# Optimization experiments

Hardware: AMD Instinct MI355X
Metric: run time of the kernel (lower is better)

## Reference

```python
import jax, jax.numpy as jnp
import numpy as np

B, T, D, H = 8, 2048, 1024, 128  # batch, seq, input_size, head_size


def setup_inputs() -> dict:
    key = jax.random.key(0)
    kx, kq, kk, kv = jax.random.split(key, 4)
    s = 1.0 / np.sqrt(D)
    return {
        "x": jax.random.normal(kx, (B, T, D), dtype=jnp.float32),
        "Wq": jax.random.normal(kq, (D, H), dtype=jnp.float32) * s,
        "Wk": jax.random.normal(kk, (D, H), dtype=jnp.float32) * s,
        "Wv": jax.random.normal(kv, (D, H), dtype=jnp.float32) * s,
    }


def reference(x, Wq, Wk, Wv):
    # projections (Linear, no bias)
    q = jnp.einsum("btd,dh->bth", x, Wq)
    k = jnp.einsum("btd,dh->bth", x, Wk)
    v = jnp.einsum("btd,dh->bth", x, Wv)
    scale = H ** (-0.5)
    scores = jnp.einsum("bth,bsh->bts", q, k) * scale  # [B,T,T]
    t = x.shape[1]
    causal = jnp.tril(jnp.ones((t, t), dtype=bool))
    scores = jnp.where(causal, scores, -jnp.inf)
    attn = jax.nn.softmax(scores, axis=-1)  # dropout p=0.0 -> identity
    out = jnp.einsum("bts,bsh->bth", attn, v)
    return out
```

## Files before the change

### kernel.cpp

```cpp
#include <hip/hip_runtime.h>
#include <math.h>

#define B_ 8
#define T_ 2048
#define D_ 1024
#define H_ 128
#define BT (B_ * T_)

typedef short bf16x8 __attribute__((ext_vector_type(8)));
typedef float f32x4 __attribute__((ext_vector_type(4)));

static constexpr float SCALE = 0.08838834764831845f;

__device__ inline unsigned short f2b(float f) {
  unsigned int u = __float_as_uint(f);
  u += 0x7FFF + ((u >> 16) & 1);
  return (unsigned short)(u >> 16);
}
__device__ inline unsigned int pk2(float a, float b) {
  return (unsigned int)f2b(a) | ((unsigned int)f2b(b) << 16);
}

__device__ __forceinline__ void gll16(const void* g, void* l) {
  __builtin_amdgcn_global_load_lds(
      (const __attribute__((address_space(1))) void*)g,
      (__attribute__((address_space(3))) void*)l, 16, 0, 0);
}

__global__ __launch_bounds__(256) void wcvt_kernel(
    const float* __restrict__ Wq, const float* __restrict__ Wk,
    const float* __restrict__ Wv, short* __restrict__ Wt) {
  __shared__ short Wls[128 * 72];
  const int sel = blockIdx.y;
  const float* W = sel == 0 ? Wq : (sel == 1 ? Wk : Wv);
  const int d0 = blockIdx.x * 64;
  const int tid = threadIdx.x;
#pragma unroll
  for (int i = 0; i < 8; ++i) {
    int slot = tid + i * 256;
    int r = slot >> 5, hg = slot & 31;
    float4 w = *(const float4*)(W + (size_t)(d0 + r) * H_ + hg * 4);
    Wls[(hg * 4 + 0) * 72 + r] = (short)f2b(w.x);
    Wls[(hg * 4 + 1) * 72 + r] = (short)f2b(w.y);
    Wls[(hg * 4 + 2) * 72 + r] = (short)f2b(w.z);
    Wls[(hg * 4 + 3) * 72 + r] = (short)f2b(w.w);
  }
  __syncthreads();
  short* dst = Wt + (size_t)sel * D_ * H_;
#pragma unroll
  for (int i = 0; i < 4; ++i) {
    int slot = tid + i * 256;
    int h = slot >> 3, g = slot & 7;
    *(int4*)(dst + (size_t)h * D_ + d0 + g * 8) = *(int4*)&Wls[h * 72 + g * 8];
  }
}

__global__ __launch_bounds__(256) void proj_kernel(
    const float* __restrict__ x, const short* __restrict__ Wt,
    short* __restrict__ qb, short* __restrict__ kb, short* __restrict__ vtb) {
  __shared__ alignas(16) char smem[36864];
  short* Xs = (short*)smem;
  short* Ws = (short*)(smem + 16384);

  const int tid = threadIdx.x;
  const int wave = tid >> 6, lane = tid & 63;
  const int ln = lane & 15, quad = lane >> 4;
  const int mw = wave & 1, nw = wave >> 1;
  const int sel = blockIdx.y;
  const int row0 = blockIdx.x * 128;
  const short* W = Wt + (size_t)sel * (size_t)(D_ * H_);

  f32x4 acc[4][4];
#pragma unroll
  for (int mi = 0; mi < 4; ++mi)
#pragma unroll
    for (int ni = 0; ni < 4; ++ni) acc[mi][ni] = (f32x4){0.f, 0.f, 0.f, 0.f};

  for (int s = 0; s < 16; ++s) {
    const int k0 = s * 64;
    if (s) __syncthreads();

#pragma unroll
    for (int j = 0; j < 4; ++j) {
      const int rbase = wave * 32 + j * 8;
      const int n = rbase + (lane >> 3);
      const int gp = (lane & 7) ^ (n & 7);
      gll16(W + (size_t)n * D_ + k0 + gp * 8, (char*)Ws + rbase * 128);
    }
    {
      float4 xr[8];
#pragma unroll
      for (int i = 0; i < 8; ++i) {
        int fid = tid + i * 256;
        int r = fid >> 4, g4 = fid & 15;
        xr[i] = *(const float4*)(x + (size_t)(row0 + r) * D_ + k0 + g4 * 4);
      }
#pragma unroll
      for (int i = 0; i < 8; ++i) {
        int fid = tid + i * 256;
        int r = fid >> 4, g4 = fid & 15;
        int g = g4 >> 1, half = g4 & 1;
        unsigned int* p = (unsigned int*)&Xs[r * 64 + ((g ^ (r & 7)) * 8) + half * 4];
        p[0] = pk2(xr[i].x, xr[i].y);
        p[1] = pk2(xr[i].z, xr[i].w);
      }
    }
    __syncthreads();

#pragma unroll
    for (int kk = 0; kk < 2; ++kk) {
      bf16x8 a[4];
#pragma unroll
      for (int mi = 0; mi < 4; ++mi) {
        int r = mw * 64 + mi * 16 + ln;
        int g = kk * 4 + quad;
        a[mi] = *(bf16x8*)&Xs[r * 64 + ((g ^ (r & 7)) * 8)];
      }
#pragma unroll
      for (int ni = 0; ni < 4; ++ni) {
        int n = nw * 64 + ni * 16 + ln;
        int g = kk * 4 + quad;
        bf16x8 bb = *(bf16x8*)&Ws[n * 64 + ((g ^ (n & 7)) * 8)];
#pragma unroll
        for (int mi = 0; mi < 4; ++mi)
          acc[mi][ni] = __builtin_amdgcn_mfma_f32_16x16x32_bf16(a[mi], bb, acc[mi][ni], 0, 0, 0);
      }
    }
  }

  __syncthreads();
  short* Cs = (short*)smem;
  if (sel < 2) {
    short* out = sel ? kb : qb;
#pragma unroll
    for (int mi = 0; mi < 4; ++mi)
#pragma unroll
      for (int ni = 0; ni < 4; ++ni)
#pragma unroll
        for (int rr = 0; rr < 4; ++rr)
          Cs[(mw * 64 + mi * 16 + quad * 4 + rr) * 136 + nw * 64 + ni * 16 + ln] =
              (short)f2b(acc[mi][ni][rr]);
    __syncthreads();
#pragma unroll
    for (int i = 0; i < 8; ++i) {
      int slot = tid + i * 256;
      int r = slot >> 4, g = slot & 15;
      *(int4*)(out + (size_t)(row0 + r) * H_ + g * 8) = *(int4*)&Cs[r * 136 + g * 8];
    }
  } else {
#pragma unroll
    for (int mi = 0; mi < 4; ++mi)
#pragma unroll
      for (int ni = 0; ni < 4; ++ni)
#pragma unroll
        for (int rr = 0; rr < 4; ++rr)
          Cs[(nw * 64 + ni * 16 + ln) * 136 + mw * 64 + mi * 16 + quad * 4 + rr] =
              (short)f2b(acc[mi][ni][rr]);
    __syncthreads();
    const int b = row0 >> 11, t0 = row0 & 2047;
#pragma unroll
    for (int i = 0; i < 8; ++i) {
      int slot = tid + i * 256;
      int h = slot >> 4, g = slot & 15;
      *(int4*)(vtb + (size_t)(b * H_ + h) * T_ + t0 + g * 8) = *(int4*)&Cs[h * 136 + g * 8];
    }
  }
}

__global__ __launch_bounds__(256) void attn_kernel(
    const short* __restrict__ qb, const short* __restrict__ kb,
    const short* __restrict__ vtb, float* __restrict__ out) {
  __shared__ alignas(16) short Ks[2][64 * 128];
  __shared__ alignas(16) short Vt[2][128 * 64];
  __shared__ alignas(16) float Sf[32 * 65];
  __shared__ alignas(16) short P[32 * 72];
  __shared__ float aA[32], lL[32];

  const int tid = threadIdx.x;
  const int wave = tid >> 6, lane = tid & 63;
  const int ln = lane & 15, quad = lane >> 4;
  const int slot = blockIdx.x & 255;
  const int pass = blockIdx.x >> 8;
  const int b = slot >> 5;
  const int j = slot & 31;
  const int tile = pass ? (63 - j) : j;
  const int q0 = tile * 32;

  bf16x8 qfr[2][4];
#pragma unroll
  for (int m = 0; m < 2; ++m)
#pragma unroll
    for (int kk = 0; kk < 4; ++kk)
      qfr[m][kk] = *(const bf16x8*)(qb + (size_t)(b * T_ + q0 + m * 16 + ln) * H_ +
                                    kk * 32 + quad * 8);

  f32x4 oacc[2][2];
#pragma unroll
  for (int m = 0; m < 2; ++m)
#pragma unroll
    for (int nt = 0; nt < 2; ++nt) oacc[m][nt] = (f32x4){0.f, 0.f, 0.f, 0.f};

  const int srow = tid >> 3, l8 = tid & 7;
  float m_run = -INFINITY, l_run = 0.f;

  auto stage = [&](int bf, int s0) {
#pragma unroll
    for (int jj = 0; jj < 4; ++jj) {
      const int rb = wave * 16 + jj * 4;
      const int r = rb + (lane >> 4);
      const int gp = (lane & 15) ^ (r & 7);
      gll16(kb + (size_t)(b * T_ + s0 + r) * H_ + gp * 8,
            (char*)&Ks[bf][0] + rb * 256);
    }
#pragma unroll
    for (int jj = 0; jj < 4; ++jj) {
      const int hb = wave * 32 + jj * 8;
      const int h = hb + (lane >> 3);
      const int gp = (lane & 7) ^ (h & 7);
      gll16(vtb + (size_t)(b * H_ + h) * T_ + s0 + gp * 8,
            (char*)&Vt[bf][0] + hb * 128);
    }
  };

  const int nch = ((q0 + 31) >> 6) + 1;
  stage(0, 0);

  for (int ch = 0; ch < nch; ++ch) {
    const int cur = ch & 1;
    const int s0 = ch * 64;
    __syncthreads();
    if (ch + 1 < nch) stage(cur ^ 1, s0 + 64);

    f32x4 sacc[2];
    sacc[0] = (f32x4){0.f, 0.f, 0.f, 0.f};
    sacc[1] = (f32x4){0.f, 0.f, 0.f, 0.f};
#pragma unroll
    for (int kk = 0; kk < 4; ++kk) {
      const int r = wave * 16 + ln;
      bf16x8 bk = *(bf16x8*)&Ks[cur][r * 128 + (((kk * 4 + quad) ^ (r & 7)) * 8)];
#pragma unroll
      for (int m = 0; m < 2; ++m)
        sacc[m] = __builtin_amdgcn_mfma_f32_16x16x32_bf16(qfr[m][kk], bk, sacc[m], 0, 0, 0);
    }
#pragma unroll
    for (int m = 0; m < 2; ++m)
#pragma unroll
      for (int r = 0; r < 4; ++r)
        Sf[(m * 16 + quad * 4 + r) * 65 + wave * 16 + ln] = sacc[m][r];
    __syncthreads();

    float sv[8];
    const int qg = q0 + srow;
#pragma unroll
    for (int i = 0; i < 8; ++i) {
      float s = Sf[srow * 65 + l8 * 8 + i] * SCALE;
      sv[i] = (s0 + l8 * 8 + i <= qg) ? s : -INFINITY;
    }
    float mx = sv[0];
#pragma unroll
    for (int i = 1; i < 8; ++i) mx = fmaxf(mx, sv[i]);
    mx = fmaxf(mx, __shfl_xor(mx, 1));
    mx = fmaxf(mx, __shfl_xor(mx, 2));
    mx = fmaxf(mx, __shfl_xor(mx, 4));
    const float mnew = fmaxf(m_run, mx);
    const float alpha = __expf(m_run - mnew);
    float p[8], ps = 0.f;
#pragma unroll
    for (int i = 0; i < 8; ++i) {
      p[i] = __expf(sv[i] - mnew);
      ps += p[i];
    }
    ps += __shfl_xor(ps, 1);
    ps += __shfl_xor(ps, 2);
    ps += __shfl_xor(ps, 4);
    l_run = l_run * alpha + ps;
    m_run = mnew;
    int4 pw;
    pw.x = (int)pk2(p[0], p[1]);
    pw.y = (int)pk2(p[2], p[3]);
    pw.z = (int)pk2(p[4], p[5]);
    pw.w = (int)pk2(p[6], p[7]);
    *(int4*)&P[srow * 72 + l8 * 8] = pw;
    if (l8 == 0) aA[srow] = alpha;
    __syncthreads();

    const int h0 = wave * 32;
    float ar[2][4];
#pragma unroll
    for (int m = 0; m < 2; ++m)
#pragma unroll
      for (int r = 0; r < 4; ++r) ar[m][r] = aA[m * 16 + quad * 4 + r];
#pragma unroll
    for (int m = 0; m < 2; ++m)
#pragma unroll
      for (int nt = 0; nt < 2; ++nt)
#pragma unroll
        for (int r = 0; r < 4; ++r) oacc[m][nt][r] *= ar[m][r];
#pragma unroll
    for (int ks = 0; ks < 2; ++ks) {
      bf16x8 pa[2];
      pa[0] = *(bf16x8*)&P[ln * 72 + ks * 32 + quad * 8];
      pa[1] = *(bf16x8*)&P[(16 + ln) * 72 + ks * 32 + quad * 8];
#pragma unroll
      for (int nt = 0; nt < 2; ++nt) {
        const int n = h0 + nt * 16 + ln;
        bf16x8 bv = *(bf16x8*)&Vt[cur][n * 64 + (((ks * 4 + quad) ^ (n & 7)) * 8)];
#pragma unroll
        for (int m = 0; m < 2; ++m)
          oacc[m][nt] = __builtin_amdgcn_mfma_f32_16x16x32_bf16(pa[m], bv, oacc[m][nt], 0, 0, 0);
      }
    }
  }

  if (l8 == 0) lL[srow] = l_run;
  __syncthreads();
  const int h0 = wave * 32;
#pragma unroll
  for (int m = 0; m < 2; ++m) {
    float linv[4];
#pragma unroll
    for (int r = 0; r < 4; ++r) linv[r] = 1.f / lL[m * 16 + quad * 4 + r];
#pragma unroll
    for (int nt = 0; nt < 2; ++nt)
#pragma unroll
      for (int r = 0; r < 4; ++r) {
        int row = q0 + m * 16 + quad * 4 + r;
        out[(size_t)(b * T_ + row) * H_ + h0 + nt * 16 + ln] = oacc[m][nt][r] * linv[r];
      }
  }
}

extern "C" void kernel_launch(void* const* d_in, const int* in_sizes, int n_in,
                              void* d_out, int out_size, void* d_ws, size_t ws_size,
                              hipStream_t stream) {
  const float* x  = (const float*)d_in[0];
  const float* Wq = (const float*)d_in[1];
  const float* Wk = (const float*)d_in[2];
  const float* Wv = (const float*)d_in[3];
  float* out = (float*)d_out;

  char* ws = (char*)d_ws;
  short* qb  = (short*)(ws);
  short* kb  = (short*)(ws + 4194304);
  short* vtb = (short*)(ws + 8388608);
  short* Wt  = (short*)(ws + 12582912);

  wcvt_kernel<<<dim3(D_ / 64, 3), 256, 0, stream>>>(Wq, Wk, Wv, Wt);
  proj_kernel<<<dim3(BT / 128, 3), 256, 0, stream>>>(x, Wt, qb, kb, vtb);
  attn_kernel<<<dim3(8 * 64), 256, 0, stream>>>(qb, kb, vtb, out);
}
```

Before: 180.1 us.

## Restructure attention to 2 waves each owning 16 query rows with register softmax

Rewrites the attention kernel so each of two waves owns 16 query rows across all 128 head dims. S is computed transposed (K as A operand), which lets the softmax max and sum run in registers with cross-lane shuffles instead of going through a shared score buffer with extra barriers. The output is staged through LDS so global stores are coalesced float4 writes. The trade-offs are half as many threads per block, V no longer double-buffered (staged each chunk after the barrier), and more accumulator registers per wave.

```diff
diff --git a/kernel.cpp b/kernel.cpp
--- a/kernel.cpp
+++ b/kernel.cpp
@@ -167,17 +167,17 @@
   }
 }
 
-__global__ __launch_bounds__(256) void attn_kernel(
+__global__ __launch_bounds__(128) void attn_kernel(
     const short* __restrict__ qb, const short* __restrict__ kb,
     const short* __restrict__ vtb, float* __restrict__ out) {
-  __shared__ alignas(16) short Ks[2][64 * 128];
-  __shared__ alignas(16) short Vt[2][128 * 64];
-  __shared__ alignas(16) float Sf[32 * 65];
-  __shared__ alignas(16) short P[32 * 72];
-  __shared__ float aA[32], lL[32];
+  __shared__ alignas(16) char smem[53632];
+  short* Ks0 = (short*)smem;
+  short* Ks1 = (short*)(smem + 16384);
+  short* Vt  = (short*)(smem + 32768);
+  short* Pt  = (short*)(smem + 49152);
 
   const int tid = threadIdx.x;
-  const int wave = tid >> 6, lane = tid & 63;
+  const int wv = tid >> 6, lane = tid & 63;
   const int ln = lane & 15, quad = lane >> 4;
   const int slot = blockIdx.x & 255;
   const int pass = blockIdx.x >> 8;
@@ -186,147 +186,136 @@
   const int tile = pass ? (63 - j) : j;
   const int q0 = tile * 32;
 
-  bf16x8 qfr[2][4];
-#pragma unroll
-  for (int m = 0; m < 2; ++m)
-#pragma unroll
-    for (int kk = 0; kk < 4; ++kk)
-      qfr[m][kk] = *(const bf16x8*)(qb + (size_t)(b * T_ + q0 + m * 16 + ln) * H_ +
-                                    kk * 32 + quad * 8);
-
-  f32x4 oacc[2][2];
-#pragma unroll
-  for (int m = 0; m < 2; ++m)
-#pragma unroll
-    for (int nt = 0; nt < 2; ++nt) oacc[m][nt] = (f32x4){0.f, 0.f, 0.f, 0.f};
-
-  const int srow = tid >> 3, l8 = tid & 7;
+  short* myP = Pt + wv * (16 * 68);
+
+  bf16x8 qfr[4];
+#pragma unroll
+  for (int kk = 0; kk < 4; ++kk)
+    qfr[kk] = *(const bf16x8*)(qb + (size_t)(b * T_ + q0 + wv * 16 + ln) * H_ +
+                               kk * 32 + quad * 8);
+
+  f32x4 oacc[8];
+#pragma unroll
+  for (int ht = 0; ht < 8; ++ht) oacc[ht] = (f32x4){0.f, 0.f, 0.f, 0.f};
+
   float m_run = -INFINITY, l_run = 0.f;
-
-  auto stage = [&](int bf, int s0) {
-#pragma unroll
-    for (int jj = 0; jj < 4; ++jj) {
-      const int rb = wave * 16 + jj * 4;
+  const int qglob = q0 + wv * 16 + ln;
+
+  auto stageK = [&](short* dst, int s0) {
+#pragma unroll
+    for (int jj = 0; jj < 8; ++jj) {
+      const int rb = wv * 32 + jj * 4;
       const int r = rb + (lane >> 4);
       const int gp = (lane & 15) ^ (r & 7);
-      gll16(kb + (size_t)(b * T_ + s0 + r) * H_ + gp * 8,
-            (char*)&Ks[bf][0] + rb * 256);
-    }
-#pragma unroll
-    for (int jj = 0; jj < 4; ++jj) {
-      const int hb = wave * 32 + jj * 8;
+      gll16(kb + (size_t)(b * T_ + s0 + r) * H_ + gp * 8, (char*)dst + rb * 256);
+    }
+  };
+  auto stageV = [&](int s0) {
+#pragma unroll
+    for (int jj = 0; jj < 8; ++jj) {
+      const int hb = wv * 64 + jj * 8;
       const int h = hb + (lane >> 3);
       const int gp = (lane & 7) ^ (h & 7);
-      gll16(vtb + (size_t)(b * H_ + h) * T_ + s0 + gp * 8,
-            (char*)&Vt[bf][0] + hb * 128);
+      gll16(vtb + (size_t)(b * H_ + h) * T_ + s0 + gp * 8, (char*)Vt + hb * 128);
     }
   };
 
-  const int nch = ((q0 + 31) >> 6) + 1;
-  stage(0, 0);
+  const int nch = (q0 >> 6) + 1;
+  stageK(Ks0, 0);
 
   for (int ch = 0; ch < nch; ++ch) {
-    const int cur = ch & 1;
     const int s0 = ch * 64;
-    __syncthreads();
-    if (ch + 1 < nch) stage(cur ^ 1, s0 + 64);
-
-    f32x4 sacc[2];
-    sacc[0] = (f32x4){0.f, 0.f, 0.f, 0.f};
-    sacc[1] = (f32x4){0.f, 0.f, 0.f, 0.f};
+    short* Kc = (ch & 1) ? Ks1 : Ks0;
+    __syncthreads();
+    stageV(s0);
+    if (ch + 1 < nch) stageK((ch & 1) ? Ks0 : Ks1, s0 + 64);
+
+    f32x4 sacc[4];
+#pragma unroll
+    for (int t = 0; t < 4; ++t) sacc[t] = (f32x4){0.f, 0.f, 0.f, 0.f};
 #pragma unroll
     for (int kk = 0; kk < 4; ++kk) {
-      const int r = wave * 16 + ln;
-      bf16x8 bk = *(bf16x8*)&Ks[cur][r * 128 + (((kk * 4 + quad) ^ (r & 7)) * 8)];
-#pragma unroll
-      for (int m = 0; m < 2; ++m)
-        sacc[m] = __builtin_amdgcn_mfma_f32_16x16x32_bf16(qfr[m][kk], bk, sacc[m], 0, 0, 0);
-    }
-#pragma unroll
-    for (int m = 0; m < 2; ++m)
-#pragma unroll
-      for (int r = 0; r < 4; ++r)
-        Sf[(m * 16 + quad * 4 + r) * 65 + wave * 16 + ln] = sacc[m][r];
-    __syncthreads();
-
-    float sv[8];
-    const int qg = q0 + srow;
-#pragma unroll
-    for (int i = 0; i < 8; ++i) {
-      float s = Sf[srow * 65 + l8 * 8 + i] * SCALE;
-      sv[i] = (s0 + l8 * 8 + i <= qg) ? s : -INFINITY;
-    }
-    float mx = sv[0];
-#pragma unroll
-    for (int i = 1; i < 8; ++i) mx = fmaxf(mx, sv[i]);
-    mx = fmaxf(mx, __shfl_xor(mx, 1));
-    mx = fmaxf(mx, __shfl_xor(mx, 2));
-    mx = fmaxf(mx, __shfl_xor(mx, 4));
-    const float mnew = fmaxf(m_run, mx);
+#pragma unroll
+      for (int t = 0; t < 4; ++t) {
+        const int krow = t * 16 + ln;
+        bf16x8 kf = *(bf16x8*)&Kc[krow * 128 + (((kk * 4 + quad) ^ (ln & 7)) * 8)];
+        sacc[t] = __builtin_amdgcn_mfma_f32_16x16x32_bf16(kf, qfr[kk], sacc[t], 0, 0, 0);
+      }
+    }
+
+    float sv[4][4];
+    float mc = -INFINITY;
+#pragma unroll
+    for (int t = 0; t < 4; ++t)
+#pragma unroll
+      for (int r = 0; r < 4; ++r) {
+        const int key = s0 + t * 16 + quad * 4 + r;
+        float s = sacc[t][r] * SCALE;
+        sv[t][r] = (key <= qglob) ? s : -INFINITY;
+        mc = fmaxf(mc, sv[t][r]);
+      }
+    mc = fmaxf(mc, __shfl_xor(mc, 16));
+    mc = fmaxf(mc, __shfl_xor(mc, 32));
+    const float mnew = fmaxf(m_run, mc);
     const float alpha = __expf(m_run - mnew);
-    float p[8], ps = 0.f;
-#pragma unroll
-    for (int i = 0; i < 8; ++i) {
-      p[i] = __expf(sv[i] - mnew);
-      ps += p[i];
-    }
-    ps += __shfl_xor(ps, 1);
-    ps += __shfl_xor(ps, 2);
-    ps += __shfl_xor(ps, 4);
-    l_run = l_run * alpha + ps;
+    float lc = 0.f;
+    float p[4][4];
+#pragma unroll
+    for (int t = 0; t < 4; ++t)
+#pragma unroll
+      for (int r = 0; r < 4; ++r) {
+        p[t][r] = __expf(sv[t][r] - mnew);
+        lc += p[t][r];
+      }
+    lc += __shfl_xor(lc, 16);
+    lc += __shfl_xor(lc, 32);
+    l_run = l_run * alpha + lc;
     m_run = mnew;
-    int4 pw;
-    pw.x = (int)pk2(p[0], p[1]);
-    pw.y = (int)pk2(p[2], p[3]);
-    pw.z = (int)pk2(p[4], p[5]);
-    pw.w = (int)pk2(p[6], p[7]);
-    *(int4*)&P[srow * 72 + l8 * 8] = pw;
-    if (l8 == 0) aA[srow] = alpha;
-    __syncthreads();
-
-    const int h0 = wave * 32;
-    float ar[2][4];
-#pragma unroll
-    for (int m = 0; m < 2; ++m)
-#pragma unroll
-      for (int r = 0; r < 4; ++r) ar[m][r] = aA[m * 16 + quad * 4 + r];
-#pragma unroll
-    for (int m = 0; m < 2; ++m)
-#pragma unroll
-      for (int nt = 0; nt < 2; ++nt)
-#pragma unroll
-        for (int r = 0; r < 4; ++r) oacc[m][nt][r] *= ar[m][r];
-#pragma unroll
-    for (int ks = 0; ks < 2; ++ks) {
-      bf16x8 pa[2];
-      pa[0] = *(bf16x8*)&P[ln * 72 + ks * 32 + quad * 8];
-      pa[1] = *(bf16x8*)&P[(16 + ln) * 72 + ks * 32 + quad * 8];
-#pragma unroll
-      for (int nt = 0; nt < 2; ++nt) {
-        const int n = h0 + nt * 16 + ln;
-        bf16x8 bv = *(bf16x8*)&Vt[cur][n * 64 + (((ks * 4 + quad) ^ (n & 7)) * 8)];
-#pragma unroll
-        for (int m = 0; m < 2; ++m)
-          oacc[m][nt] = __builtin_amdgcn_mfma_f32_16x16x32_bf16(pa[m], bv, oacc[m][nt], 0, 0, 0);
-      }
-    }
-  }
-
-  if (l8 == 0) lL[srow] = l_run;
+
+#pragma unroll
+    for (int t = 0; t < 4; ++t) {
+      *(unsigned int*)&myP[ln * 68 + t * 16 + quad * 4 + 0] = pk2(p[t][0], p[t][1]);
+      *(unsigned int*)&myP[ln * 68 + t * 16 + quad * 4 + 2] = pk2(p[t][2], p[t][3]);
+    }
+#pragma unroll
+    for (int ht = 0; ht < 8; ++ht)
+#pragma unroll
+      for (int r = 0; r < 4; ++r) oacc[ht][r] *= alpha;
+
+    __syncthreads();
+
+#pragma unroll
+    for (int kk2 = 0; kk2 < 2; ++kk2) {
+      bf16x8 pf = *(bf16x8*)&myP[ln * 68 + kk2 * 32 + quad * 8];
+#pragma unroll
+      for (int ht = 0; ht < 8; ++ht) {
+        const int hrow = ht * 16 + ln;
+        bf16x8 vf = *(bf16x8*)&Vt[hrow * 64 + (((kk2 * 4 + quad) ^ (ln & 7)) * 8)];
+        oacc[ht] = __builtin_amdgcn_mfma_f32_16x16x32_bf16(vf, pf, oacc[ht], 0, 0, 0);
+      }
+    }
+  }
+
+  const float linv = 1.0f / l_run;
+#pragma unroll
+  for (int ht = 0; ht < 8; ++ht)
+#pragma unroll
+    for (int r = 0; r < 4; ++r) oacc[ht][r] *= linv;
+
   __syncthreads();
-  const int h0 = wave * 32;
-#pragma unroll
-  for (int m = 0; m < 2; ++m) {
-    float linv[4];
-#pragma unroll
-    for (int r = 0; r < 4; ++r) linv[r] = 1.f / lL[m * 16 + quad * 4 + r];
-#pragma unroll
-    for (int nt = 0; nt < 2; ++nt)
-#pragma unroll
-      for (int r = 0; r < 4; ++r) {
-        int row = q0 + m * 16 + quad * 4 + r;
-        out[(size_t)(b * T_ + row) * H_ + h0 + nt * 16 + ln] = oacc[m][nt][r] * linv[r];
-      }
+  float* Ot = (float*)smem;
+#pragma unroll
+  for (int ht = 0; ht < 8; ++ht) {
+    double2* dst = (double2*)&Ot[(wv * 16 + ln) * 132 + ht * 16 + quad * 4];
+    *(double2*)dst = *(double2*)&oacc[ht];
+  }
+  __syncthreads();
+#pragma unroll
+  for (int i = 0; i < 8; ++i) {
+    int slot2 = tid + i * 128;
+    int r = slot2 >> 5, c = slot2 & 31;
+    float4 v = *(float4*)&Ot[r * 132 + c * 4];
+    *(float4*)(out + (size_t)(b * T_ + q0 + r) * H_ + c * 4) = v;
   }
 }
 
@@ -347,5 +336,5 @@
 
   wcvt_kernel<<<dim3(D_ / 64, 3), 256, 0, stream>>>(Wq, Wk, Wv, Wt);
   proj_kernel<<<dim3(BT / 128, 3), 256, 0, stream>>>(x, Wt, qb, kb, vtb);
-  attn_kernel<<<dim3(8 * 64), 256, 0, stream>>>(qb, kb, vtb, out);
-}
+  attn_kernel<<<dim3(512), 128, 0, stream>>>(qb, kb, vtb, out);
+}
```

Result: no change. 176.6 us (-1.9%).
